# Optimization experiments

Measured on AMD Instinct MI355X. Metric: run time of the kernel, lower is better.

Reference implementation:

```python
import jax, jax.numpy as jnp
import numpy as np

B, T, S, A = 8, 256, 16, 1
H, NH, L, NI, TIME, TMAX = 1024, 16, 6, 4096, 8, 512
NEG = -10000.0


def _ln(x, g, b, eps=1e-5):
    m = jnp.mean(x, -1, keepdims=True)
    v = jnp.mean((x - m) ** 2, -1, keepdims=True)
    return (x - m) * jax.lax.rsqrt(v + eps) * g + b


def setup_inputs() -> dict:
    key = jax.random.key(0)
    ks = iter(jax.random.split(key, 64))
    w = lambda *s: 0.02 * jax.random.normal(next(ks), s, jnp.float32)
    inp = {
        'states': jax.random.normal(next(ks), (B, T, S), jnp.float32),
        'actions': jax.random.normal(next(ks), (B, T, A), jnp.float32),
        'rtgs': jax.random.normal(next(ks), (B, T, 1), jnp.float32),
        'attention_mask': jnp.ones((B, T, 1), jnp.float32),
        'state_mean': jnp.zeros((S,), jnp.float32),
        'state_std': jnp.ones((S,), jnp.float32),
        'W_es': w(S, H), 'b_es': jnp.zeros((H,)),
        'W_ea': w(A, H), 'b_ea': jnp.zeros((H,)),
        'W_er': w(1, H), 'b_er': jnp.zeros((H,)),
        'E_t': w(TMAX, TIME),
        'W_ts': w(H + TIME, H), 'b_ts': jnp.zeros((H,)),
        'W_ta': w(H + TIME, H), 'b_ta': jnp.zeros((H,)),
        'W_tr': w(H + TIME, H), 'b_tr': jnp.zeros((H,)),
        'eln_g': jnp.ones((H,)), 'eln_b': jnp.zeros((H,)),
        'ln1_g': jnp.ones((L, H)), 'ln1_b': jnp.zeros((L, H)),
        'ln2_g': jnp.ones((L, H)), 'ln2_b': jnp.zeros((L, H)),
        'Wq': w(L, H, H), 'bq': jnp.zeros((L, H)),
        'Wk': w(L, H, H), 'bk': jnp.zeros((L, H)),
        'Wv': w(L, H, H), 'bv': jnp.zeros((L, H)),
        'Wo': w(L, H, H), 'bo': jnp.zeros((L, H)),
        'W1': w(L, H, NI), 'b1': jnp.zeros((L, NI)),
        'W2': w(L, NI, H), 'b2': jnp.zeros((L, H)),
        'W_pa': w(H, A), 'b_pa': jnp.zeros((A,)),
        'timesteps': jax.random.randint(next(ks), (B, T), 0, TMAX),
    }
    return inp


def _forward(states, actions, rtgs, attention_mask, state_mean, state_std,
             W_es, b_es, W_ea, b_ea, W_er, b_er, E_t,
             W_ts, b_ts, W_ta, b_ta, W_tr, b_tr, eln_g, eln_b,
             ln1_g, ln1_b, ln2_g, ln2_b, Wq, bq, Wk, bk, Wv, bv, Wo, bo,
             W1, b1, W2, b2, W_pa, b_pa, timesteps):
    T3 = 3 * T
    dh = H // NH
    s = (states - state_mean) / (state_std + 1e-9)
    te = E_t[timesteps]                                   # [B,T,8]
    se = jnp.concatenate([s @ W_es + b_es, te], -1) @ W_ts + b_ts
    ae = jnp.concatenate([actions @ W_ea + b_ea, te], -1) @ W_ta + b_ta
    re = jnp.concatenate([rtgs @ W_er + b_er, te], -1) @ W_tr + b_tr
    # interleave (rtg, state, action) per timestep -> [B, 3T, H]
    x = jnp.stack([re, se, ae], axis=2).reshape(B, T3, H)
    x = _ln(x, eln_g, eln_b)

    timestep_mask = jnp.max(attention_mask, axis=-1)      # [B,T]
    pad = (1.0 - jnp.repeat(timestep_mask, 3, axis=1)) * NEG  # [B,3T]
    pad = pad[:, None, None, :]
    causal = jnp.tril(jnp.ones((T3, T3), bool))

    def block(x, p):
        (l1g, l1b, wq, bqv, wk, bkv, wv, bvv, wo, bov,
         l2g, l2b, w1, b1v, w2, b2v) = p
        h = _ln(x, l1g, l1b)
        def heads(w, b):
            return (h @ w + b).reshape(B, T3, NH, dh).transpose(0, 2, 1, 3)
        q, k, v = heads(wq, bqv), heads(wk, bkv), heads(wv, bvv)
        att = jnp.einsum('bhqd,bhkd->bhqk', q, k) / jnp.sqrt(jnp.float32(dh))
        att = jnp.where(causal, att, jnp.asarray(NEG, att.dtype)) + pad
        att = jax.nn.softmax(att, axis=-1)
        y = jnp.einsum('bhqk,bhkd->bhqd', att, v)
        y = y.transpose(0, 2, 1, 3).reshape(B, T3, H) @ wo + bov
        x = x + y
        m = _ln(x, l2g, l2b)
        x = x + jax.nn.gelu(m @ w1 + b1v, approximate=False) @ w2 + b2v
        return x, None

    stacked = (ln1_g, ln1_b, Wq, bq, Wk, bk, Wv, bv, Wo, bo,
               ln2_g, ln2_b, W1, b1, W2, b2)
    x, _ = jax.lax.scan(block, x, stacked)

    x = x.reshape(B, T, 3, H)
    action_preds = x[:, :, 1] @ W_pa + b_pa               # state-token positions
    return action_preds


def reference(states, actions, rtgs, attention_mask, state_mean, state_std,
              W_es, b_es, W_ea, b_ea, W_er, b_er, E_t,
              W_ts, b_ts, W_ta, b_ta, W_tr, b_tr, eln_g, eln_b,
              ln1_g, ln1_b, ln2_g, ln2_b, Wq, bq, Wk, bk, Wv, bv, Wo, bo,
              W1, b1, W2, b2, W_pa, b_pa, timesteps):
    return _forward(states, actions, rtgs, attention_mask, state_mean, state_std,
                    W_es, b_es, W_ea, b_ea, W_er, b_er, E_t,
                    W_ts, b_ts, W_ta, b_ta, W_tr, b_tr, eln_g, eln_b,
                    ln1_g, ln1_b, ln2_g, ln2_b, Wq, bq, Wk, bk, Wv, bv, Wo, bo,
                    W1, b1, W2, b2, W_pa, b_pa, timesteps)
```

## Files before the change

### kernel.cpp

```cpp
#include <hip/hip_runtime.h>
#include <math.h>

#define B_    8
#define T_    256
#define S_    16
#define H_    1024
#define NH_   16
#define L_    6
#define NI_   4096
#define TIME_ 8
#define T3_   768
#define DH_   64
#define BT_   2048
#define ROWS_ 6144
#define KE_   1032
#define KEP_  1056
#define NEGV  (-10000.0f)

typedef unsigned short u16;
typedef short bf16x8 __attribute__((ext_vector_type(8)));
typedef float f32x4 __attribute__((ext_vector_type(4)));

__device__ __forceinline__ float bf2f(u16 u) {
    union { unsigned int i; float f; } x; x.i = ((unsigned int)u) << 16; return x.f;
}
__device__ __forceinline__ u16 f2bf(float f) {
    union { float f; unsigned int i; } x; x.f = f;
    unsigned int r = x.i + 0x7FFFu + ((x.i >> 16) & 1u);
    return (u16)(r >> 16);
}
__device__ __forceinline__ float gelu_fast(float x) {
    float y = 0.7978845608028654f * (x + 0.044715f * x * x * x);
    float e = __expf(2.0f * y);
    float t = 1.0f - 2.0f / (e + 1.0f);
    return 0.5f * x * (1.0f + t);
}

__device__ __forceinline__ void gll16(const u16* g, u16* l) {
    __builtin_amdgcn_global_load_lds(
        (const __attribute__((address_space(1))) unsigned int*)g,
        (__attribute__((address_space(3))) unsigned int*)l,
        16, 0, 0);
}

template <int EPI, int BM>
__device__ __forceinline__ void mgemm_core(
    const u16* __restrict__ A, const u16* __restrict__ Bt,
    const float* __restrict__ bias, float* __restrict__ outf,
    u16* __restrict__ outb, const float* __restrict__ res,
    int N, int K, int koff, int klen, bool addb)
{
    constexpr int MT = (BM == 128) ? 4 : 2;
    __shared__ u16 Als[2][BM * 32];
    __shared__ u16 Bls[2][128 * 32];
    const int tid = threadIdx.x;

    const int nbx = N >> 7;
    const int bid = blockIdx.x;
    const int G = nbx << 3;
    const int grp = bid / G;
    const int g = bid - grp * G;
    const int bm = (grp * 8 + (g & 7)) * BM;
    const int bn = (g >> 3) * 128;

    const int lane = tid & 63;
    const int w = tid >> 6;
    const int wr = (BM == 128) ? (w >> 1) : (w & 1);
    const int wc = (BM == 128) ? (w & 1) : (w >> 1);
    const int lrow = lane & 15;
    const int lk = lane >> 4;

    f32x4 acc[MT][4] = {};

    auto stage = [&](int buf, int kk) {
        if (BM == 128) {
            #pragma unroll
            for (int s = 0; s < 2; ++s) {
                const int gb = w * 64 + s * 256;
                const int j = gb >> 7, m0 = gb & 127;
                gll16(A + (size_t)(bm + m0 + lane) * K + kk + j * 8, Als[buf] + gb * 8);
            }
        } else {
            gll16(A + (size_t)(bm + lane) * K + kk + w * 8, Als[buf] + w * 64 * 8);
        }
        #pragma unroll
        for (int s = 0; s < 2; ++s) {
            const int gb = w * 64 + s * 256;
            const int j = gb >> 7, m0 = gb & 127;
            gll16(Bt + (size_t)(bn + m0 + lane) * K + kk + j * 8, Bls[buf] + gb * 8);
        }
    };

    const int niter = klen >> 5;
    stage(0, koff);
    for (int i = 0; i < niter; ++i) {
        __syncthreads();
        if (i + 1 < niter) stage((i + 1) & 1, koff + (i + 1) * 32);
        const bf16x8* Af = (const bf16x8*)Als[i & 1];
        const bf16x8* Bf = (const bf16x8*)Bls[i & 1];
        bf16x8 af[MT], bfr[4];
        #pragma unroll
        for (int tm = 0; tm < MT; ++tm)
            af[tm] = Af[lk * BM + wr * (MT * 16) + tm * 16 + lrow];
        #pragma unroll
        for (int tn = 0; tn < 4; ++tn)
            bfr[tn] = Bf[lk * 128 + wc * 64 + tn * 16 + lrow];
        #pragma unroll
        for (int tm = 0; tm < MT; ++tm)
            #pragma unroll
            for (int tn = 0; tn < 4; ++tn)
                acc[tm][tn] = __builtin_amdgcn_mfma_f32_16x16x32_bf16(
                    af[tm], bfr[tn], acc[tm][tn], 0, 0, 0);
    }

    int cg[4]; float bv[4];
    #pragma unroll
    for (int tn = 0; tn < 4; ++tn) {
        cg[tn] = bn + wc * 64 + tn * 16 + lrow;
        bv[tn] = addb ? bias[cg[tn]] : 0.0f;
    }
    #pragma unroll
    for (int tm = 0; tm < MT; ++tm) {
        const int rbase = bm + wr * (MT * 16) + tm * 16 + lk * 4;
        #pragma unroll
        for (int r = 0; r < 4; ++r) {
            const size_t rowoff = (size_t)(rbase + r) * N;
            #pragma unroll
            for (int tn = 0; tn < 4; ++tn) {
                float v = acc[tm][tn][r] + bv[tn];
                const size_t idx = rowoff + cg[tn];
                if (EPI == 0) outf[idx] = v;
                else if (EPI == 1) outf[idx] = v + res[idx];
                else if (EPI == 2) outb[idx] = f2bf(v);
                else if (EPI == 3) { outb[idx] = f2bf(gelu_fast(v)); }
                else { unsafeAtomicAdd(outf + idx, v); }
            }
        }
    }
}

template <int EPI, int BM>
__global__ __launch_bounds__(256) void mgemm(
    const u16* __restrict__ A, const u16* __restrict__ Bt,
    const float* __restrict__ bias, float* __restrict__ outf,
    u16* __restrict__ outb, const float* __restrict__ res,
    int N, int K)
{
    mgemm_core<EPI, BM>(A, Bt, bias, outf, outb, res, N, K, 0, K, true);
}

template <int EPI, int BM>
__global__ __launch_bounds__(256) void mgemm_sk(
    const u16* __restrict__ A, const u16* __restrict__ Bt,
    const float* __restrict__ bias, float* __restrict__ outf,
    u16* __restrict__ outb, const float* __restrict__ res,
    int N, int K, int nsplit)
{
    const int split = blockIdx.y;
    const int klen = K / nsplit;
    mgemm_core<EPI, BM>(A, Bt, bias, outf, outb, res, N, K,
                        split * klen, klen, split == 0);
}

__global__ __launch_bounds__(256) void mgemm_embed(
    const u16* __restrict__ U, const u16* __restrict__ Wt,
    const float* __restrict__ b0, const float* __restrict__ b1,
    const float* __restrict__ b2, float* __restrict__ out)
{
    const int z = blockIdx.z;
    const float* bias = (z == 0) ? b0 : (z == 1) ? b1 : b2;
    mgemm_core<0, 64>(U + (size_t)z * BT_ * KEP_, Wt + (size_t)z * H_ * KEP_,
                      bias, out + (size_t)z * BT_ * H_, nullptr, nullptr,
                      H_, KEP_, 0, KEP_, true);
}

__device__ __forceinline__ void convT_core(
    const float* __restrict__ W, u16* __restrict__ Wt,
    int K, int N, int Kpad, int bx, int by)
{
    __shared__ float tile[32][65];
    const int k0 = by * 32, n0 = bx * 64;
    const int tid = threadIdx.x;
    #pragma unroll
    for (int p = 0; p < 2; ++p) {
        const int kr = (tid >> 4) + p * 16;
        const int nc = (tid & 15) * 4;
        const int k = k0 + kr;
        float4 v = make_float4(0.f, 0.f, 0.f, 0.f);
        if (k < K) v = *(const float4*)(W + (size_t)k * N + n0 + nc);
        tile[kr][nc + 0] = v.x; tile[kr][nc + 1] = v.y;
        tile[kr][nc + 2] = v.z; tile[kr][nc + 3] = v.w;
    }
    __syncthreads();
    #pragma unroll
    for (int p = 0; p < 2; ++p) {
        const int idx = tid + p * 256;
        const int n = idx >> 3, kq = (idx & 7) * 4;
        ushort4 o;
        o.x = f2bf(tile[kq + 0][n]); o.y = f2bf(tile[kq + 1][n]);
        o.z = f2bf(tile[kq + 2][n]); o.w = f2bf(tile[kq + 3][n]);
        *(ushort4*)(Wt + (size_t)(n0 + n) * Kpad + k0 + kq) = o;
    }
}

__global__ __launch_bounds__(256) void convT_layer(
    const float* __restrict__ Wq, const float* __restrict__ Wk,
    const float* __restrict__ Wv, const float* __restrict__ Wo,
    const float* __restrict__ W1, const float* __restrict__ W2,
    const float* __restrict__ bq, const float* __restrict__ bk,
    const float* __restrict__ bv,
    u16* __restrict__ WQKVt, u16* __restrict__ Wot,
    u16* __restrict__ W1t, u16* __restrict__ W2t, float* __restrict__ bqkv)
{
    const int bid = blockIdx.x;
    const int seg = bid >> 11, r = bid & 2047;
    if (seg == 0) {
        const int z = r >> 9, rr = r & 511;
        const int bx = rr & 15, by = rr >> 4;
        const float* W = (z == 0) ? Wq : (z == 1) ? Wk : (z == 2) ? Wv : Wo;
        u16* Wt = (z == 3) ? Wot : WQKVt + (size_t)z * H_ * H_;
        convT_core(W, Wt, H_, H_, H_, bx, by);
        if (bx == 0 && by == 0 && z < 3) {
            const float* bsrc = (z == 0) ? bq : (z == 1) ? bk : bv;
            #pragma unroll
            for (int u = 0; u < 4; ++u) {
                int i = threadIdx.x + u * 256;
                bqkv[z * H_ + i] = bsrc[i];
            }
        }
    } else if (seg == 1) {
        const int bx = r & 63, by = r >> 6;
        convT_core(W1, W1t, H_, NI_, H_, bx, by);
    } else {
        const int bx = r & 15, by = r >> 4;
        convT_core(W2, W2t, NI_, H_, NI_, bx, by);
    }
}

__global__ __launch_bounds__(256) void convT_embed(
    const float* __restrict__ W0, const float* __restrict__ W1,
    const float* __restrict__ W2, u16* __restrict__ Wt)
{
    const int z = blockIdx.z;
    const float* W = (z == 0) ? W0 : (z == 1) ? W1 : W2;
    convT_core(W, Wt + (size_t)z * H_ * KEP_, KE_, H_, KEP_, blockIdx.x, blockIdx.y);
}

__global__ __launch_bounds__(256) void embed_pre_kernel(
    const float* __restrict__ states, const float* __restrict__ actions,
    const float* __restrict__ rtgs, const float* __restrict__ mean,
    const float* __restrict__ stdv, const float* __restrict__ W_es,
    const float* __restrict__ b_es, const float* __restrict__ W_ea,
    const float* __restrict__ b_ea, const float* __restrict__ W_er,
    const float* __restrict__ b_er, const float* __restrict__ E_t,
    const int* __restrict__ timesteps,
    u16* __restrict__ Us, u16* __restrict__ Ua, u16* __restrict__ Ur)
{
    const int bt  = blockIdx.x;
    const int tid = threadIdx.x;
    __shared__ float sn[S_];
    __shared__ float tev[TIME_];
    if (tid < S_) sn[tid] = (states[bt * S_ + tid] - mean[tid]) / (stdv[tid] + 1e-9f);
    if (tid < TIME_) {
        int ts = timesteps[bt];
        tev[tid] = E_t[ts * TIME_ + tid];
    }
    __syncthreads();
    const float av = actions[bt];
    const float rv = rtgs[bt];
    const size_t rowo = (size_t)bt * KEP_;
    #pragma unroll
    for (int u = 0; u < 4; ++u) {
        int n = tid + u * 256;
        float accs = b_es[n];
        #pragma unroll
        for (int i = 0; i < S_; ++i) accs += sn[i] * W_es[i * H_ + n];
        Us[rowo + n] = f2bf(accs);
        Ua[rowo + n] = f2bf(av * W_ea[n] + b_ea[n]);
        Ur[rowo + n] = f2bf(rv * W_er[n] + b_er[n]);
    }
    if (tid < TIME_) {
        u16 tv = f2bf(tev[tid]);
        Us[rowo + H_ + tid] = tv;
        Ua[rowo + H_ + tid] = tv;
        Ur[rowo + H_ + tid] = tv;
    }
    if (tid < KEP_ - KE_) {
        Us[rowo + KE_ + tid] = 0;
        Ua[rowo + KE_ + tid] = 0;
        Ur[rowo + KE_ + tid] = 0;
    }
}

template <bool BF16OUT>
__device__ __forceinline__ void ln_body(const float* __restrict__ src,
                                        const float* __restrict__ g,
                                        const float* __restrict__ b,
                                        void* __restrict__ dst,
                                        float* red, int tid)
{
    float v[4];
    #pragma unroll
    for (int u = 0; u < 4; ++u) v[u] = src[tid + u * 256];
    float s = v[0] + v[1] + v[2] + v[3];
    red[tid] = s; __syncthreads();
    for (int off = 128; off > 0; off >>= 1) {
        if (tid < off) red[tid] += red[tid + off];
        __syncthreads();
    }
    const float mean = red[0] * (1.0f / H_);
    __syncthreads();
    float ss = 0.0f;
    #pragma unroll
    for (int u = 0; u < 4; ++u) { float d = v[u] - mean; ss += d * d; }
    red[tid] = ss; __syncthreads();
    for (int off = 128; off > 0; off >>= 1) {
        if (tid < off) red[tid] += red[tid + off];
        __syncthreads();
    }
    const float var = red[0] * (1.0f / H_);
    const float rs = rsqrtf(var + 1e-5f);
    #pragma unroll
    for (int u = 0; u < 4; ++u) {
        int col = tid + u * 256;
        float y = (v[u] - mean) * rs * g[col] + b[col];
        if (BF16OUT) ((u16*)dst)[col] = f2bf(y);
        else ((float*)dst)[col] = y;
    }
}

__global__ __launch_bounds__(256) void ln_bf16_kernel(
    const float* __restrict__ X, const float* __restrict__ g,
    const float* __restrict__ b, u16* __restrict__ Y)
{
    __shared__ float red[256];
    const size_t row = blockIdx.x;
    ln_body<true>(X + row * H_, g, b, Y + row * H_, red, threadIdx.x);
}

__global__ __launch_bounds__(256) void interleave_eln_kernel(
    const float* __restrict__ RE, const float* __restrict__ SE,
    const float* __restrict__ AE, const float* __restrict__ g,
    const float* __restrict__ b, float* __restrict__ X)
{
    __shared__ float red[256];
    const int row = blockIdx.x;
    const int bi = row / T3_;
    const int rem = row % T3_;
    const int t = rem / 3, slot = rem % 3;
    const float* src = (slot == 0 ? RE : (slot == 1 ? SE : AE)) + (size_t)(bi * T_ + t) * H_;
    ln_body<false>(src, g, b, X + (size_t)row * H_, red, threadIdx.x);
}

__global__ __launch_bounds__(256) void attn_kernel(
    const u16* __restrict__ QKV, const float* __restrict__ amask,
    u16* __restrict__ Y)
{
    const int qt = blockIdx.x;
    const int h  = blockIdx.y;
    const int b  = blockIdx.z;
    const int tid = threadIdx.x;
    const int lane = tid & 63, w = tid >> 6;
    const int l15 = lane & 15, quad = lane >> 4;

    __shared__ u16 Kls[64][72];
    __shared__ u16 Vt[64][72];
    __shared__ u16 Pls[4][16][72];
    __shared__ float padv[64];

    const u16* Qbase = QKV + (size_t)b * T3_ * 3072 + h * 64;
    const u16* Kbase = Qbase + 1024;
    const u16* Vbase = Qbase + 2048;

    bf16x8 qf[2];
    {
        const u16* qp = Qbase + (size_t)(qt * 64 + w * 16 + l15) * 3072 + quad * 8;
        qf[0] = *(const bf16x8*)qp;
        qf[1] = *(const bf16x8*)(qp + 32);
    }

    float m_i[4], l_i[4];
    f32x4 o[4] = {};
    #pragma unroll
    for (int r = 0; r < 4; ++r) { m_i[r] = -3.0e30f; l_i[r] = 0.0f; }

    const int qr0 = qt * 64 + w * 16 + quad * 4;

    for (int kt = 0; kt <= qt; ++kt) {
        #pragma unroll
        for (int s = 0; s < 2; ++s) {
            const int c = tid + s * 256;
            const int tok = c >> 3, cb = c & 7;
            const size_t go = (size_t)(kt * 64 + tok) * 3072 + cb * 8;
            *(uint4*)&Kls[tok][cb * 8] = *(const uint4*)(Kbase + go);
            uint4 vv = *(const uint4*)(Vbase + go);
            const u16* vs = (const u16*)&vv;
            #pragma unroll
            for (int j = 0; j < 8; ++j) Vt[cb * 8 + j][tok] = vs[j];
        }
        if (tid < 64)
            padv[tid] = (1.0f - amask[b * T_ + (kt * 64 + tid) / 3]) * NEGV;
        __syncthreads();

        f32x4 sacc[4];
        #pragma unroll
        for (int nt = 0; nt < 4; ++nt) {
            bf16x8 kf0 = *(const bf16x8*)&Kls[nt * 16 + l15][quad * 8];
            bf16x8 kf1 = *(const bf16x8*)&Kls[nt * 16 + l15][32 + quad * 8];
            f32x4 z = {};
            z = __builtin_amdgcn_mfma_f32_16x16x32_bf16(qf[0], kf0, z, 0, 0, 0);
            sacc[nt] = __builtin_amdgcn_mfma_f32_16x16x32_bf16(qf[1], kf1, z, 0, 0, 0);
        }

        float sv[4][4];
        float rmax[4] = {-3.0e30f, -3.0e30f, -3.0e30f, -3.0e30f};
        #pragma unroll
        for (int nt = 0; nt < 4; ++nt) {
            const int jc = kt * 64 + nt * 16 + l15;
            const float pv = padv[nt * 16 + l15];
            #pragma unroll
            for (int r = 0; r < 4; ++r) {
                float v = (jc <= qr0 + r) ? sacc[nt][r] * 0.125f : NEGV;
                v += pv;
                sv[nt][r] = v;
                rmax[r] = fmaxf(rmax[r], v);
            }
        }
        #pragma unroll
        for (int m = 1; m < 16; m <<= 1)
            #pragma unroll
            for (int r = 0; r < 4; ++r)
                rmax[r] = fmaxf(rmax[r], __shfl_xor(rmax[r], m, 64));
        float al[4], rsum[4];
        #pragma unroll
        for (int r = 0; r < 4; ++r) {
            const float mn = fmaxf(m_i[r], rmax[r]);
            al[r] = __expf(m_i[r] - mn);
            m_i[r] = mn;
            float sum = 0.0f;
            #pragma unroll
            for (int nt = 0; nt < 4; ++nt) {
                float p = __expf(sv[nt][r] - mn);
                sv[nt][r] = p; sum += p;
            }
            rsum[r] = sum;
        }
        #pragma unroll
        for (int m = 1; m < 16; m <<= 1)
            #pragma unroll
            for (int r = 0; r < 4; ++r)
                rsum[r] += __shfl_xor(rsum[r], m, 64);
        #pragma unroll
        for (int r = 0; r < 4; ++r)
            l_i[r] = l_i[r] * al[r] + rsum[r];

        #pragma unroll
        for (int nt = 0; nt < 4; ++nt)
            #pragma unroll
            for (int r = 0; r < 4; ++r)
                Pls[w][quad * 4 + r][nt * 16 + l15] = f2bf(sv[nt][r]);
        #pragma unroll
        for (int dt = 0; dt < 4; ++dt)
            #pragma unroll
            for (int r = 0; r < 4; ++r)
                o[dt][r] *= al[r];

        bf16x8 pf0 = *(const bf16x8*)&Pls[w][l15][quad * 8];
        bf16x8 pf1 = *(const bf16x8*)&Pls[w][l15][32 + quad * 8];
        #pragma unroll
        for (int dt = 0; dt < 4; ++dt) {
            bf16x8 vf0 = *(const bf16x8*)&Vt[dt * 16 + l15][quad * 8];
            bf16x8 vf1 = *(const bf16x8*)&Vt[dt * 16 + l15][32 + quad * 8];
            o[dt] = __builtin_amdgcn_mfma_f32_16x16x32_bf16(pf0, vf0, o[dt], 0, 0, 0);
            o[dt] = __builtin_amdgcn_mfma_f32_16x16x32_bf16(pf1, vf1, o[dt], 0, 0, 0);
        }
        __syncthreads();
    }

    #pragma unroll
    for (int r = 0; r < 4; ++r) {
        const float inv = 1.0f / l_i[r];
        const size_t row = (size_t)b * T3_ + qt * 64 + w * 16 + quad * 4 + r;
        #pragma unroll
        for (int dt = 0; dt < 4; ++dt)
            Y[row * H_ + h * 64 + dt * 16 + l15] = f2bf(o[dt][r] * inv);
    }
}

__global__ __launch_bounds__(256) void head_kernel(
    const float* __restrict__ X, const float* __restrict__ W_pa,
    const float* __restrict__ b_pa, float* __restrict__ out)
{
    __shared__ float red[256];
    const int row = blockIdx.x;
    const int b = row / T_, t = row % T_;
    const float* x = X + ((size_t)b * T3_ + 3 * t + 1) * H_;
    const int tid = threadIdx.x;
    float s = 0.0f;
    #pragma unroll
    for (int u = 0; u < 4; ++u) {
        int col = tid + u * 256;
        s += x[col] * W_pa[col];
    }
    red[tid] = s; __syncthreads();
    for (int off = 128; off > 0; off >>= 1) {
        if (tid < off) red[tid] += red[tid + off];
        __syncthreads();
    }
    if (tid == 0) out[row] = red[0] + b_pa[0];
}

extern "C" void kernel_launch(void* const* d_in, const int* in_sizes, int n_in,
                              void* d_out, int out_size, void* d_ws, size_t ws_size,
                              hipStream_t stream)
{
    const float* states  = (const float*)d_in[0];
    const float* actions = (const float*)d_in[1];
    const float* rtgs    = (const float*)d_in[2];
    const float* amask   = (const float*)d_in[3];
    const float* smean   = (const float*)d_in[4];
    const float* sstd    = (const float*)d_in[5];
    const float* W_es    = (const float*)d_in[6];
    const float* b_es    = (const float*)d_in[7];
    const float* W_ea    = (const float*)d_in[8];
    const float* b_ea    = (const float*)d_in[9];
    const float* W_er    = (const float*)d_in[10];
    const float* b_er    = (const float*)d_in[11];
    const float* E_t     = (const float*)d_in[12];
    const float* W_ts    = (const float*)d_in[13];
    const float* b_ts    = (const float*)d_in[14];
    const float* W_ta    = (const float*)d_in[15];
    const float* b_ta    = (const float*)d_in[16];
    const float* W_tr    = (const float*)d_in[17];
    const float* b_tr    = (const float*)d_in[18];
    const float* eln_g   = (const float*)d_in[19];
    const float* eln_b   = (const float*)d_in[20];
    const float* ln1_g   = (const float*)d_in[21];
    const float* ln1_b   = (const float*)d_in[22];
    const float* ln2_g   = (const float*)d_in[23];
    const float* ln2_b   = (const float*)d_in[24];
    const float* Wq      = (const float*)d_in[25];
    const float* bq      = (const float*)d_in[26];
    const float* Wk      = (const float*)d_in[27];
    const float* bk      = (const float*)d_in[28];
    const float* Wv      = (const float*)d_in[29];
    const float* bv      = (const float*)d_in[30];
    const float* Wo      = (const float*)d_in[31];
    const float* bo      = (const float*)d_in[32];
    const float* W1      = (const float*)d_in[33];
    const float* b1      = (const float*)d_in[34];
    const float* W2      = (const float*)d_in[35];
    const float* b2      = (const float*)d_in[36];
    const float* W_pa    = (const float*)d_in[37];
    const float* b_pa    = (const float*)d_in[38];
    const int*   tsteps  = (const int*)d_in[39];
    float* out = (float*)d_out;

    char* base = (char*)d_ws;
    float* X    = (float*)base;
    u16*   Hb   = (u16*)(base + 25165824);
    u16*   QKVb = (u16*)(base + 37748736);
    u16*   MIDb = (u16*)(base + 75497472);
    u16*   Wbuf = (u16*)(base + 125829120);

    float* bqkv = (float*)MIDb;
    u16* U_s = MIDb;
    u16* U_a = MIDb + (size_t)BT_ * KEP_;
    u16* U_r = MIDb + (size_t)2 * BT_ * KEP_;
    float* SE = (float*)QKVb;
    float* AE = SE + (size_t)BT_ * H_;
    float* RE = AE + (size_t)BT_ * H_;
    u16* Wemb = Wbuf;

    u16* WQKVt = Wbuf;
    u16* Wot   = Wbuf + (size_t)3072 * 1024;
    u16* W1t   = Wbuf + (size_t)4096 * 1024;
    u16* W2t   = Wbuf + (size_t)8192 * 1024;

    embed_pre_kernel<<<BT_, 256, 0, stream>>>(
        states, actions, rtgs, smean, sstd, W_es, b_es, W_ea, b_ea,
        W_er, b_er, E_t, tsteps, U_s, U_a, U_r);

    dim3 gCvE(H_ / 64, KEP_ / 32, 3);
    convT_embed<<<gCvE, 256, 0, stream>>>(W_ts, W_ta, W_tr, Wemb);

    dim3 gEmb((H_ / 128) * (BT_ / 64), 1, 3);
    mgemm_embed<<<gEmb, 256, 0, stream>>>(U_s, Wemb, b_ts, b_ta, b_tr, SE);

    interleave_eln_kernel<<<ROWS_, 256, 0, stream>>>(RE, SE, AE, eln_g, eln_b, X);

    const int gQKV = (3072 / 128) * (ROWS_ / 128);
    const int gO   = (H_ / 128) * (ROWS_ / 128);
    const int gM1  = (NI_ / 128) * (ROWS_ / 128);
    dim3 gF2sk((H_ / 128) * (ROWS_ / 128), 4);
    dim3 gAttn(T3_ / 64, NH_, B_);

    for (int l = 0; l < L_; ++l) {
        const size_t wOff = (size_t)l * H_ * H_;
        const size_t bOff = (size_t)l * H_;
        const size_t w1Off = (size_t)l * H_ * NI_;
        const size_t b1Off = (size_t)l * NI_;

        convT_layer<<<6144, 256, 0, stream>>>(
            Wq + wOff, Wk + wOff, Wv + wOff, Wo + wOff,
            W1 + w1Off, W2 + w1Off,
            bq + bOff, bk + bOff, bv + bOff,
            WQKVt, Wot, W1t, W2t, bqkv);

        ln_bf16_kernel<<<ROWS_, 256, 0, stream>>>(X, ln1_g + bOff, ln1_b + bOff, Hb);
        mgemm<2, 128><<<gQKV, 256, 0, stream>>>(Hb, WQKVt, bqkv, nullptr, QKVb, nullptr, 3072, H_);
        attn_kernel<<<gAttn, 256, 0, stream>>>(QKVb, amask, Hb);
        mgemm<1, 128><<<gO, 256, 0, stream>>>(Hb, Wot, bo + bOff, X, nullptr, X, H_, H_);
        ln_bf16_kernel<<<ROWS_, 256, 0, stream>>>(X, ln2_g + bOff, ln2_b + bOff, Hb);
        mgemm<3, 128><<<gM1, 256, 0, stream>>>(Hb, W1t, b1 + b1Off, nullptr, MIDb, nullptr, NI_, H_);
        mgemm_sk<4, 128><<<gF2sk, 256, 0, stream>>>(MIDb, W2t, b2 + bOff, X, nullptr, nullptr, H_, NI_, 4);
    }

    head_kernel<<<BT_, 256, 0, stream>>>(X, W_pa, b_pa, out);
}
```

Before: 3.274 ms.

## Add 256x256 swizzled pipelined GEMM kernel for all transformer layer matmuls

Introduces a 512-thread GEMM with 256x256 output tiles, K-step 64, XOR-swizzled LDS layout, a 128KB double buffer, staged half-tile prefetch interleaved with MFMA phases, and setprio around the MFMA phases. It replaces the 128x128 kernels for QKV, O-proj, FFN1 and FFN2, and drops FFN2 split-K atomics in favour of a single-pass residual epilogue. The intent is higher data reuse and better overlap of loads with compute. The cost is lower occupancy, and small grids such as 96 blocks for O-proj and FFN2 may underfill the 256 CUs.

Measured after the change: 2.809 ms. 14.2% less time.

```diff
diff --git a/kernel.cpp b/kernel.cpp
--- a/kernel.cpp
+++ b/kernel.cpp
@@ -43,12 +43,176 @@
         16, 0, 0);
 }
 
+template <int EPI>
+__global__ __launch_bounds__(512) void mgemm256(
+    const u16* __restrict__ A, const u16* __restrict__ Bt,
+    const float* __restrict__ bias, float* __restrict__ outf,
+    u16* __restrict__ outb, const float* __restrict__ res,
+    int N, int K)
+{
+    extern __shared__ u16 smem[];
+    const int tid  = threadIdx.x;
+    const int lane = tid & 63, w = tid >> 6;
+    const int l15  = lane & 15, quad = lane >> 4;
+    const int wm   = w >> 2, wn = w & 3;
+
+    const int nbx = N >> 8;
+    const int bid = blockIdx.x;
+    const int G   = nbx << 3;
+    const int grp = bid / G;
+    const int g   = bid - grp * G;
+    const int bm  = (grp * 8 + (g & 7)) * 256;
+    const int bn  = (g >> 3) * 256;
+
+    const int NT = K >> 6;
+
+    auto stageHT = [&](int t, int ht) {
+        u16* lbase = smem + (t & 1) * 32768 + ((ht & 2) ? 16384 : 0);
+        const u16* gsrc = (ht & 2) ? Bt : A;
+        const int rb = (ht & 2) ? bn : bm;
+        const int k0 = t << 6;
+        const int h  = ht & 1;
+        #pragma unroll
+        for (int s = 0; s < 2; ++s) {
+            const int gb = h * 8192 + s * 4096 + w * 512;
+            const int p  = (gb + lane * 8) * 2;
+            const int lin = p ^ (((p >> 7) & 7) << 4);
+            const int row = lin >> 7;
+            const int cu  = (lin & 127) >> 1;
+            gll16(gsrc + (size_t)(rb + row) * K + k0 + cu, lbase + gb);
+        }
+    };
+
+    f32x4 acc[8][4] = {};
+
+    stageHT(0, 0); stageHT(0, 1); stageHT(0, 2); stageHT(0, 3);
+    stageHT(1, 0); stageHT(1, 1);
+    asm volatile("s_waitcnt vmcnt(4)" ::: "memory");
+    __builtin_amdgcn_s_barrier();
+
+    const int swz = (l15 & 7) << 4;
+
+    for (int t = 0; t < NT; ++t) {
+        const u16* Ab = smem + (t & 1) * 32768;
+        const u16* Bb = Ab + 16384;
+        bf16x8 a0[4][2], a1[4][2], b0[2][2], b1[2][2];
+
+        #pragma unroll
+        for (int f = 0; f < 4; ++f)
+            #pragma unroll
+            for (int ks = 0; ks < 2; ++ks)
+                a0[f][ks] = *(const bf16x8*)((const char*)Ab +
+                    (wm * 128 + f * 16 + l15) * 128 + ((ks * 64 + quad * 16) ^ swz));
+        #pragma unroll
+        for (int n = 0; n < 2; ++n)
+            #pragma unroll
+            for (int ks = 0; ks < 2; ++ks)
+                b0[n][ks] = *(const bf16x8*)((const char*)Bb +
+                    (wn * 64 + n * 16 + l15) * 128 + ((ks * 64 + quad * 16) ^ swz));
+        if (t + 1 < NT) stageHT(t + 1, 2);
+        __builtin_amdgcn_s_barrier();
+        __builtin_amdgcn_s_setprio(1);
+        #pragma unroll
+        for (int f = 0; f < 4; ++f)
+            #pragma unroll
+            for (int n = 0; n < 2; ++n)
+                #pragma unroll
+                for (int ks = 0; ks < 2; ++ks)
+                    acc[f][n] = __builtin_amdgcn_mfma_f32_16x16x32_bf16(
+                        a0[f][ks], b0[n][ks], acc[f][n], 0, 0, 0);
+        __builtin_amdgcn_s_setprio(0);
+        __builtin_amdgcn_s_barrier();
+
+        #pragma unroll
+        for (int f = 0; f < 4; ++f)
+            #pragma unroll
+            for (int ks = 0; ks < 2; ++ks)
+                a1[f][ks] = *(const bf16x8*)((const char*)Ab +
+                    (64 + wm * 128 + f * 16 + l15) * 128 + ((ks * 64 + quad * 16) ^ swz));
+        if (t + 1 < NT) stageHT(t + 1, 3);
+        __builtin_amdgcn_s_barrier();
+        __builtin_amdgcn_s_setprio(1);
+        #pragma unroll
+        for (int f = 0; f < 4; ++f)
+            #pragma unroll
+            for (int n = 0; n < 2; ++n)
+                #pragma unroll
+                for (int ks = 0; ks < 2; ++ks)
+                    acc[4 + f][n] = __builtin_amdgcn_mfma_f32_16x16x32_bf16(
+                        a1[f][ks], b0[n][ks], acc[4 + f][n], 0, 0, 0);
+        __builtin_amdgcn_s_setprio(0);
+        __builtin_amdgcn_s_barrier();
+
+        #pragma unroll
+        for (int n = 0; n < 2; ++n)
+            #pragma unroll
+            for (int ks = 0; ks < 2; ++ks)
+                b1[n][ks] = *(const bf16x8*)((const char*)Bb +
+                    (32 + wn * 64 + n * 16 + l15) * 128 + ((ks * 64 + quad * 16) ^ swz));
+        if (t + 2 < NT) stageHT(t + 2, 0);
+        __builtin_amdgcn_s_barrier();
+        __builtin_amdgcn_s_setprio(1);
+        #pragma unroll
+        for (int f = 0; f < 4; ++f)
+            #pragma unroll
+            for (int n = 0; n < 2; ++n)
+                #pragma unroll
+                for (int ks = 0; ks < 2; ++ks)
+                    acc[f][2 + n] = __builtin_amdgcn_mfma_f32_16x16x32_bf16(
+                        a0[f][ks], b1[n][ks], acc[f][2 + n], 0, 0, 0);
+        __builtin_amdgcn_s_setprio(0);
+        __builtin_amdgcn_s_barrier();
+
+        if (t + 2 < NT) {
+            stageHT(t + 2, 1);
+            asm volatile("s_waitcnt vmcnt(4)" ::: "memory");
+        } else {
+            asm volatile("s_waitcnt vmcnt(0)" ::: "memory");
+        }
+        __builtin_amdgcn_s_barrier();
+        __builtin_amdgcn_s_setprio(1);
+        #pragma unroll
+        for (int f = 0; f < 4; ++f)
+            #pragma unroll
+            for (int n = 0; n < 2; ++n)
+                #pragma unroll
+                for (int ks = 0; ks < 2; ++ks)
+                    acc[4 + f][2 + n] = __builtin_amdgcn_mfma_f32_16x16x32_bf16(
+                        a1[f][ks], b1[n][ks], acc[4 + f][2 + n], 0, 0, 0);
+        __builtin_amdgcn_s_setprio(0);
+        __builtin_amdgcn_s_barrier();
+    }
+
+    int cg[4]; float bv[4];
+    #pragma unroll
+    for (int n = 0; n < 4; ++n) {
+        cg[n] = bn + wn * 64 + n * 16 + l15;
+        bv[n] = bias[cg[n]];
+    }
+    #pragma unroll
+    for (int mf = 0; mf < 8; ++mf) {
+        const int rbase = bm + wm * 128 + mf * 16 + quad * 4;
+        #pragma unroll
+        for (int r = 0; r < 4; ++r) {
+            const size_t rowoff = (size_t)(rbase + r) * N;
+            #pragma unroll
+            for (int n = 0; n < 4; ++n) {
+                float v = acc[mf][n][r] + bv[n];
+                const size_t idx = rowoff + cg[n];
+                if (EPI == 1) outf[idx] = v + res[idx];
+                else if (EPI == 2) outb[idx] = f2bf(v);
+                else outb[idx] = f2bf(gelu_fast(v));
+            }
+        }
+    }
+}
+
 template <int EPI, int BM>
 __device__ __forceinline__ void mgemm_core(
     const u16* __restrict__ A, const u16* __restrict__ Bt,
     const float* __restrict__ bias, float* __restrict__ outf,
     u16* __restrict__ outb, const float* __restrict__ res,
-    int N, int K, int koff, int klen, bool addb)
+    int N, int K)
 {
     constexpr int MT = (BM == 128) ? 4 : 2;
     __shared__ u16 Als[2][BM * 32];
@@ -91,11 +255,11 @@
         }
     };
 
-    const int niter = klen >> 5;
-    stage(0, koff);
+    const int niter = K >> 5;
+    stage(0, 0);
     for (int i = 0; i < niter; ++i) {
         __syncthreads();
-        if (i + 1 < niter) stage((i + 1) & 1, koff + (i + 1) * 32);
+        if (i + 1 < niter) stage((i + 1) & 1, (i + 1) * 32);
         const bf16x8* Af = (const bf16x8*)Als[i & 1];
         const bf16x8* Bf = (const bf16x8*)Bls[i & 1];
         bf16x8 af[MT], bfr[4];
@@ -117,7 +281,7 @@
     #pragma unroll
     for (int tn = 0; tn < 4; ++tn) {
         cg[tn] = bn + wc * 64 + tn * 16 + lrow;
-        bv[tn] = addb ? bias[cg[tn]] : 0.0f;
+        bv[tn] = bias[cg[tn]];
     }
     #pragma unroll
     for (int tm = 0; tm < MT; ++tm) {
@@ -132,34 +296,10 @@
                 if (EPI == 0) outf[idx] = v;
                 else if (EPI == 1) outf[idx] = v + res[idx];
                 else if (EPI == 2) outb[idx] = f2bf(v);
-                else if (EPI == 3) { outb[idx] = f2bf(gelu_fast(v)); }
-                else { unsafeAtomicAdd(outf + idx, v); }
+                else { outb[idx] = f2bf(gelu_fast(v)); }
             }
         }
     }
-}
-
-template <int EPI, int BM>
-__global__ __launch_bounds__(256) void mgemm(
-    const u16* __restrict__ A, const u16* __restrict__ Bt,
-    const float* __restrict__ bias, float* __restrict__ outf,
-    u16* __restrict__ outb, const float* __restrict__ res,
-    int N, int K)
-{
-    mgemm_core<EPI, BM>(A, Bt, bias, outf, outb, res, N, K, 0, K, true);
-}
-
-template <int EPI, int BM>
-__global__ __launch_bounds__(256) void mgemm_sk(
-    const u16* __restrict__ A, const u16* __restrict__ Bt,
-    const float* __restrict__ bias, float* __restrict__ outf,
-    u16* __restrict__ outb, const float* __restrict__ res,
-    int N, int K, int nsplit)
-{
-    const int split = blockIdx.y;
-    const int klen = K / nsplit;
-    mgemm_core<EPI, BM>(A, Bt, bias, outf, outb, res, N, K,
-                        split * klen, klen, split == 0);
 }
 
 __global__ __launch_bounds__(256) void mgemm_embed(
@@ -171,7 +311,7 @@
     const float* bias = (z == 0) ? b0 : (z == 1) ? b1 : b2;
     mgemm_core<0, 64>(U + (size_t)z * BT_ * KEP_, Wt + (size_t)z * H_ * KEP_,
                       bias, out + (size_t)z * BT_ * H_, nullptr, nullptr,
-                      H_, KEP_, 0, KEP_, true);
+                      H_, KEP_);
 }
 
 __device__ __forceinline__ void convT_core(
@@ -556,6 +696,17 @@
     const int*   tsteps  = (const int*)d_in[39];
     float* out = (float*)d_out;
 
+    static bool attrset = false;
+    if (!attrset) {
+        hipFuncSetAttribute(reinterpret_cast<const void*>(mgemm256<1>),
+                            hipFuncAttributeMaxDynamicSharedMemorySize, 131072);
+        hipFuncSetAttribute(reinterpret_cast<const void*>(mgemm256<2>),
+                            hipFuncAttributeMaxDynamicSharedMemorySize, 131072);
+        hipFuncSetAttribute(reinterpret_cast<const void*>(mgemm256<3>),
+                            hipFuncAttributeMaxDynamicSharedMemorySize, 131072);
+        attrset = true;
+    }
+
     char* base = (char*)d_ws;
     float* X    = (float*)base;
     u16*   Hb   = (u16*)(base + 25165824);
@@ -589,10 +740,9 @@
 
     interleave_eln_kernel<<<ROWS_, 256, 0, stream>>>(RE, SE, AE, eln_g, eln_b, X);
 
-    const int gQKV = (3072 / 128) * (ROWS_ / 128);
-    const int gO   = (H_ / 128) * (ROWS_ / 128);
-    const int gM1  = (NI_ / 128) * (ROWS_ / 128);
-    dim3 gF2sk((H_ / 128) * (ROWS_ / 128), 4);
+    const int gQKV = (3072 / 256) * (ROWS_ / 256);
+    const int gO   = (H_ / 256) * (ROWS_ / 256);
+    const int gM1  = (NI_ / 256) * (ROWS_ / 256);
     dim3 gAttn(T3_ / 64, NH_, B_);
 
     for (int l = 0; l < L_; ++l) {
@@ -608,12 +758,12 @@
             WQKVt, Wot, W1t, W2t, bqkv);
 
         ln_bf16_kernel<<<ROWS_, 256, 0, stream>>>(X, ln1_g + bOff, ln1_b + bOff, Hb);
-        mgemm<2, 128><<<gQKV, 256, 0, stream>>>(Hb, WQKVt, bqkv, nullptr, QKVb, nullptr, 3072, H_);
+        mgemm256<2><<<gQKV, 512, 131072, stream>>>(Hb, WQKVt, bqkv, nullptr, QKVb, nullptr, 3072, H_);
         attn_kernel<<<gAttn, 256, 0, stream>>>(QKVb, amask, Hb);
-        mgemm<1, 128><<<gO, 256, 0, stream>>>(Hb, Wot, bo + bOff, X, nullptr, X, H_, H_);
+        mgemm256<1><<<gO, 512, 131072, stream>>>(Hb, Wot, bo + bOff, X, nullptr, X, H_, H_);
         ln_bf16_kernel<<<ROWS_, 256, 0, stream>>>(X, ln2_g + bOff, ln2_b + bOff, Hb);
-        mgemm<3, 128><<<gM1, 256, 0, stream>>>(Hb, W1t, b1 + b1Off, nullptr, MIDb, nullptr, NI_, H_);
-        mgemm_sk<4, 128><<<gF2sk, 256, 0, stream>>>(MIDb, W2t, b2 + bOff, X, nullptr, nullptr, H_, NI_, 4);
+        mgemm256<3><<<gM1, 512, 131072, stream>>>(Hb, W1t, b1 + b1Off, nullptr, MIDb, nullptr, NI_, H_);
+        mgemm256<1><<<gO, 512, 131072, stream>>>(MIDb, W2t, b2 + bOff, X, nullptr, X, H_, NI_);
     }
 
     head_kernel<<<BT_, 256, 0, stream>>>(X, W_pa, b_pa, out);
```
